# Optimization experiments

Hardware: AMD Instinct MI355X
Metric: run time of the kernel (lower is better)

Reference implementation:

```python
import jax, jax.numpy as jnp
import numpy as np

B, S, N, D = 4, 12, 716, 64
H = 4            # num_heads
ALPHA = 0.2      # LeakyReLU negative slope
NEG = -9e15      # mask fill value from the torch code (-9000000000000000.0)


def setup_inputs() -> dict:
    key = jax.random.key(0)
    ks = jax.random.split(key, 20)
    sc = 1.0 / np.sqrt(D)
    inputs = jax.random.normal(ks[0], (B, S, N, D), dtype=jnp.float32)
    adj = jax.random.randint(ks[1], (N, N), 0, 2).astype(jnp.int32)
    in_degree = jax.random.randint(ks[2], (N,), 0, N)
    out_degree = jax.random.randint(ks[3], (N,), 0, N)
    # embeddings with padding_idx=0 -> row 0 zeroed
    in_emb = (jax.random.normal(ks[4], (N, D)) * sc).at[0].set(0.0)
    out_emb = (jax.random.normal(ks[5], (N, D)) * sc).at[0].set(0.0)
    # GAT params
    W = jax.random.normal(ks[6], (D, D)) * sc
    a1 = jax.random.normal(ks[7], (D, 1)) * sc
    a2 = jax.random.normal(ks[8], (D, 1)) * sc
    # spatial multi-head attention params
    Wq = jax.random.normal(ks[9], (D, D)) * sc
    bq = jnp.zeros((D,))
    Wk = jax.random.normal(ks[10], (D, D)) * sc
    bk = jnp.zeros((D,))
    Wv = jax.random.normal(ks[11], (D, D)) * sc
    bv = jnp.zeros((D,))
    Wo = jax.random.normal(ks[12], (D, D)) * sc
    bo = jnp.zeros((D,))
    # pred_linear: 2D -> D
    Wp = jax.random.normal(ks[13], (2 * D, D)) * (1.0 / np.sqrt(2 * D))
    bp = jnp.zeros((D,))
    return dict(inputs=inputs, adj=adj, in_degree=in_degree, out_degree=out_degree,
                in_emb=in_emb, out_emb=out_emb, W=W, a1=a1, a2=a2,
                Wq=Wq, bq=bq, Wk=Wk, bk=bk, Wv=Wv, bv=bv, Wo=Wo, bo=bo,
                Wp=Wp, bp=bp)


def reference(inputs, adj, in_degree, out_degree, in_emb, out_emb,
              W, a1, a2, Wq, bq, Wk, bk, Wv, bv, Wo, bo, Wp, bp):
    b, s, n, d = inputs.shape
    dh = d // H
    # degree embeddings, broadcast over batch & time: [N, D]
    spatial_emb = in_emb[in_degree] + out_emb[out_degree]

    # ---- GAT, vectorized over all batch*seq samples (orig loops per sample) ----
    x = inputs.reshape(b * s, n, d)
    Wh = jnp.einsum('bnd,de->bne', x, W)                 # [BS, N, D]
    Wh1 = Wh @ a1                                        # [BS, N, 1]
    Wh2 = Wh @ a2                                        # [BS, N, 1]
    e = Wh1 + jnp.swapaxes(Wh2, 1, 2)                    # [BS, N, N]
    e = jnp.where(e > 0, e, ALPHA * e)                   # LeakyReLU
    e = jnp.where(adj[None] > 0, e, NEG)                 # adjacency mask
    attn = jax.nn.softmax(e, axis=-1)                    # softmax(dim=1) on 2D == last axis
    out1 = jax.nn.elu(attn @ Wh).reshape(b, s, n, d)     # dropout is identity in eval

    # ---- Spatial multi-head attention over nodes ----
    y = inputs + spatial_emb                             # [B, S, N, D]
    q = (y @ Wq + bq).reshape(b, s, n, H, dh)
    k = (y @ Wk + bk).reshape(b, s, n, H, dh)
    v = (y @ Wv + bv).reshape(b, s, n, H, dh)
    scores = jnp.einsum('bsnhk,bsmhk->bshnm', q, k) / jnp.sqrt(jnp.float32(dh))
    p = jax.nn.softmax(scores, axis=-1)                  # [B, S, H, N, N]
    o = jnp.einsum('bshnm,bsmhk->bsnhk', p, v).reshape(b, s, n, d)
    out2 = o @ Wo + bo

    # ---- fuse and project ----
    return jnp.concatenate([out1, out2], axis=-1) @ Wp + bp
```

## Files before the change

### kernel.cpp

```cpp
#include <hip/hip_runtime.h>
#include <hip/hip_bf16.h>

#define BN   716
#define BD   64
#define BH   4
#define BDH  16
#define BBS  48
#define NCH  23
#define NJT  45
#define QSCALE 0.3606737602f

typedef __hip_bfloat16 bf16;
typedef __attribute__((ext_vector_type(8))) short short8;
typedef __attribute__((ext_vector_type(4))) short s16x4;
typedef __attribute__((ext_vector_type(4))) float f32x4;

__device__ __forceinline__ float b2f(bf16 x){ return __bfloat162float(x); }
__device__ __forceinline__ bf16 f2b(float x){ return __float2bfloat16(x); }
__device__ __forceinline__ short bfbits(float x){
  union { bf16 h; short s; } c; c.h = __float2bfloat16(x); return c.s;
}
__device__ __forceinline__ unsigned packbf(float a, float b){
  unsigned ua = __float_as_uint(a) + 0x8000u;
  unsigned ub = __float_as_uint(b) + 0x8000u;
  return __builtin_amdgcn_perm(ub, ua, 0x07060302u);
}
__device__ __forceinline__ short8 pack8(float a,float b,float c,float d,
                                        float e,float f,float g,float h){
  short8 r; r[0]=bfbits(a); r[1]=bfbits(b); r[2]=bfbits(c); r[3]=bfbits(d);
  r[4]=bfbits(e); r[5]=bfbits(f); r[6]=bfbits(g); r[7]=bfbits(h); return r;
}
__device__ __forceinline__ float fexp2(float x){
#if __has_builtin(__builtin_amdgcn_exp2f)
  return __builtin_amdgcn_exp2f(x);
#else
  return __expf(x * 0.6931471805599453f);
#endif
}
__device__ __forceinline__ float frcp(float x){
#if __has_builtin(__builtin_amdgcn_rcpf)
  return __builtin_amdgcn_rcpf(x);
#else
  return 1.0f / x;
#endif
}

#define MFMA16(a,b,c) __builtin_amdgcn_mfma_f32_16x16x32_bf16(a,b,c,0,0,0)

#if __has_builtin(__builtin_amdgcn_mfma_f32_16x16x16_bf16)
#define HAVE_MFMA16K 1
__device__ __forceinline__ f32x4 mfma16k(s16x4 a, s16x4 b, f32x4 c){
  return __builtin_amdgcn_mfma_f32_16x16x16_bf16(a, b, c, 0, 0, 0);
}
#elif __has_builtin(__builtin_amdgcn_mfma_f32_16x16x16bf16_1k)
#define HAVE_MFMA16K 1
__device__ __forceinline__ f32x4 mfma16k(s16x4 a, s16x4 b, f32x4 c){
  return __builtin_amdgcn_mfma_f32_16x16x16bf16_1k(a, b, c, 0, 0, 0);
}
#else
#define HAVE_MFMA16K 0
#endif

__global__ __launch_bounds__(256) void k_prep(
    const int* __restrict__ adj,
    const float* __restrict__ W,  const float* __restrict__ Wq,
    const float* __restrict__ Wk, const float* __restrict__ Wv,
    const float* __restrict__ Wo, const float* __restrict__ bo,
    const float* __restrict__ Wp, const float* __restrict__ bp,
    unsigned* __restrict__ mask, bf16* __restrict__ WB,
    bf16* __restrict__ WF, float* __restrict__ bfuse)
{
  int b = blockIdx.x, t = threadIdx.x;
  if (b < 65){
    int w = b * 256 + t;
    if (w < BN * NCH){
      int row = w / NCH, wc = w - row * NCH;
      unsigned m = 0;
      int jb = wc * 32;
      for (int bb = 0; bb < 32; bb++){
        int j = jb + bb;
        if (j < BN && adj[(long)row * BN + j] > 0) m |= (1u << bb);
      }
      mask[w] = m;
    }
  } else if (b < 69){
#pragma unroll
    for (int i = 0; i < 16; i++){
      int idx = (b - 65) * 4096 + i * 256 + t;
      int n = idx >> 6, kk = idx & 63;
      const float* src = (n < 64) ? W : (n < 128) ? Wq : (n < 192) ? Wk : Wv;
      WB[idx] = f2b(src[kk * BD + (n & 63)]);
    }
  } else if (b < 101){
    int idx = (b - 69) * 256 + t;
    int n = idx >> 7, kk = idx & 127;
    float v;
    if (kk < 64){
      v = Wp[kk * BD + n];
    } else {
      v = 0.f;
      int r = kk - 64;
      for (int m = 0; m < BD; m++)
        v += Wo[r * BD + m] * Wp[(BD + m) * BD + n];
    }
    WF[idx] = f2b(v);
  } else {
    if (t < BD){
      float acc = bp[t];
      for (int m = 0; m < BD; m++)
        acc += bo[m] * Wp[(BD + m) * BD + t];
      bfuse[t] = acc;
    }
  }
}

__global__ __launch_bounds__(256) void k_proj(
    const float* __restrict__ x,
    const int* __restrict__ ind, const int* __restrict__ outd,
    const float* __restrict__ in_emb, const float* __restrict__ out_emb,
    const float* __restrict__ a1p, const float* __restrict__ a2p,
    const bf16* __restrict__ WB,
    const float* __restrict__ bq, const float* __restrict__ bk, const float* __restrict__ bv,
    bf16* __restrict__ WhS, float* __restrict__ Wh1, float2* __restrict__ EwP,
    bf16* __restrict__ Qt, bf16* __restrict__ Kt, bf16* __restrict__ Vt16)
{
  __shared__ short st[64][72];
  int bs = blockIdx.x, tile = blockIdx.y;
  int n0 = tile * 64;
  int t = threadIdx.x, w = t >> 6, lane = t & 63, quad = lane >> 4, l15 = lane & 15;
  long sb = (long)bs * BN;
  int rowi = n0 + w * 16 + l15;
  int rc = rowi < BN ? rowi : BN - 1;
  const float* xr  = x + (sb + rc) * BD;
  const float* ier = in_emb  + (long)ind [rc] * BD;
  const float* oer = out_emb + (long)outd[rc] * BD;

  f32x4 aw[4], aqkv[12];
#pragma unroll
  for (int i2 = 0; i2 < 4;  i2++) aw[i2]   = (f32x4){0,0,0,0};
#pragma unroll
  for (int i2 = 0; i2 < 12; i2++) aqkv[i2] = (f32x4){0,0,0,0};

#pragma unroll
  for (int kc = 0; kc < 2; kc++){
    int k0 = kc * 32 + quad * 8;
    float4 xa = *(const float4*)(xr  + k0);
    float4 xb = *(const float4*)(xr  + k0 + 4);
    float4 ia = *(const float4*)(ier + k0);
    float4 ib = *(const float4*)(ier + k0 + 4);
    float4 oa = *(const float4*)(oer + k0);
    float4 ob = *(const float4*)(oer + k0 + 4);
    short8 ax = pack8(xa.x, xa.y, xa.z, xa.w, xb.x, xb.y, xb.z, xb.w);
    short8 ay = pack8(xa.x+ia.x+oa.x, xa.y+ia.y+oa.y, xa.z+ia.z+oa.z, xa.w+ia.w+oa.w,
                      xb.x+ib.x+ob.x, xb.y+ib.y+ob.y, xb.z+ib.z+ob.z, xb.w+ib.w+ob.w);
#pragma unroll
    for (int nt = 0; nt < 4; nt++)
      aw[nt] = MFMA16(ax, *(const short8*)(WB + (nt*16 + l15) * BD + k0), aw[nt]);
#pragma unroll
    for (int nt = 0; nt < 12; nt++)
      aqkv[nt] = MFMA16(ay, *(const short8*)(WB + (64 + nt*16 + l15) * BD + k0), aqkv[nt]);
  }

  {
    float s1v[4] = {0,0,0,0}, s2v[4] = {0,0,0,0};
#pragma unroll
    for (int nt = 0; nt < 4; nt++){
      float a1f = a1p[nt*16 + l15], a2f = a2p[nt*16 + l15];
#pragma unroll
      for (int reg = 0; reg < 4; reg++){
        s1v[reg] += aw[nt][reg] * a1f;
        s2v[reg] += aw[nt][reg] * a2f;
      }
    }
#pragma unroll
    for (int off = 1; off < 16; off <<= 1){
#pragma unroll
      for (int reg = 0; reg < 4; reg++){
        s1v[reg] += __shfl_xor(s1v[reg], off);
        s2v[reg] += __shfl_xor(s2v[reg], off);
      }
    }
    if (l15 == 0){
#pragma unroll
      for (int reg = 0; reg < 4; reg++){
        int rr = n0 + w*16 + quad*4 + reg;
        if (rr < BN){
          Wh1[sb + rr] = s1v[reg];
          float s2 = s2v[reg];
          EwP[sb + rr] = make_float2(__expf(s2), __expf(0.2f * s2));
        }
      }
    }
  }

#pragma unroll
  for (int nt = 0; nt < 4; nt++)
    *(short4*)&st[nt*16 + l15][w*16 + quad*4] = make_short4(
        bfbits(aw[nt][0]), bfbits(aw[nt][1]), bfbits(aw[nt][2]), bfbits(aw[nt][3]));
  __syncthreads();
#pragma unroll
  for (int s = 0; s < 2; s++){
    int L = (t*2 + s) * 8;
    int kb = L & 31, d = (L >> 5) & 63, chl = L >> 11;
    int ch = tile * 2 + chl;
    if (ch < NCH)
      *(uint4*)(WhS + (((long)bs*NCH + ch)*64 + d)*32 + kb) = *(const uint4*)&st[d][chl*32 + kb];
  }
  __syncthreads();

#pragma unroll
  for (int nt = 0; nt < 4; nt++){
    float bb = bv[nt*16 + l15];
    *(short4*)&st[nt*16 + l15][w*16 + quad*4] = make_short4(
        bfbits(aqkv[8+nt][0]+bb), bfbits(aqkv[8+nt][1]+bb),
        bfbits(aqkv[8+nt][2]+bb), bfbits(aqkv[8+nt][3]+bb));
  }
  __syncthreads();
  {
    int jl = t >> 6;
    int c  = t & 15, qq = (t >> 4) & 3;
    int jt = tile * 4 + jl;
    if (jt < NJT){
#pragma unroll
      for (int h = 0; h < BH; h++){
        s16x4 v4 = *(const s16x4*)&st[h*16 + c][jl*16 + qq*4];
        *(s16x4*)(Vt16 + ((((long)bs*BH + h)*NJT + jt)*64 + (t & 63))*4) = v4;
      }
    }
  }
  __syncthreads();

#pragma unroll
  for (int nt = 0; nt < 4; nt++){
    float bb = bq[nt*16 + l15];
#pragma unroll
    for (int reg = 0; reg < 4; reg++)
      st[w*16 + quad*4 + reg][nt*16 + l15] = bfbits((aqkv[nt][reg] + bb) * QSCALE);
  }
  __syncthreads();
#pragma unroll
  for (int s = 0; s < 2; s++){
    int L = (t*2 + s) * 8;
    int kb = L & 15, nl = (L >> 4) & 63, h = L >> 10;
    int jt = tile * 4 + (nl >> 4);
    if (jt < NJT)
      *(uint4*)(Qt + ((((long)bs*BH + h)*NJT + jt)*16 + (nl&15))*16 + kb)
          = *(const uint4*)&st[nl][h*16 + kb];
  }
  __syncthreads();

#pragma unroll
  for (int nt = 0; nt < 4; nt++){
    float bb = bk[nt*16 + l15];
#pragma unroll
    for (int reg = 0; reg < 4; reg++)
      st[w*16 + quad*4 + reg][nt*16 + l15] = bfbits(aqkv[4+nt][reg] + bb);
  }
  __syncthreads();
#pragma unroll
  for (int s = 0; s < 2; s++){
    int L = (t*2 + s) * 8;
    int kb = L & 15, nl = (L >> 4) & 63, h = L >> 10;
    int jt = tile * 4 + (nl >> 4);
    if (jt < NJT)
      *(uint4*)(Kt + ((((long)bs*BH + h)*NJT + jt)*16 + (nl&15))*16 + kb)
          = *(const uint4*)&st[nl][h*16 + kb];
  }
}

__global__ __launch_bounds__(256) void k_attn(
    const float* __restrict__ Wh1, const float2* __restrict__ EwP,
    const unsigned* __restrict__ mask, const bf16* __restrict__ WhS,
    const bf16* __restrict__ Qt, const bf16* __restrict__ Kt,
    const bf16* __restrict__ Vt16,
    bf16* __restrict__ out1, bf16* __restrict__ o)
{
#if !HAVE_MFMA16K
  __shared__ short pw[4][16][48];
#endif
  int bs = blockIdx.x, yb = blockIdx.y;
  int t = threadIdx.x, w = t >> 6, lane = t & 63, quad = lane >> 4, l15 = lane & 15;
  long sb = (long)bs * BN;

  if (yb < 12){
    int rt = yb * 4 + w;
    if (rt >= NJT) return;
    int i = rt * 16 + l15;
    int ic = i < BN ? i : BN - 1;
    float e1 = Wh1[sb + ic];
    float Aa = __expf(e1), Cc = __expf(0.2f * e1);
    float invA = frcp(Aa);
    const unsigned* mrow = mask + (long)ic * NCH;
    const float2* ew = EwP + sb;

    float sl = 0.f;
    f32x4 acc0 = {0,0,0,0}, acc1 = {0,0,0,0}, acc2 = {0,0,0,0}, acc3 = {0,0,0,0};
    for (int ch = 0; ch < NCH; ch++){
      int j0 = ch * 32 + quad * 8;
      unsigned m8 = (mrow[ch] >> (quad * 8)) & 0xFFu;
      const float4* ef = (const float4*)(ew + j0);
      float4 q0 = ef[0], q1 = ef[1], q2 = ef[2], q3 = ef[3];
      float Bv[8] = {q0.x, q0.z, q1.x, q1.z, q2.x, q2.z, q3.x, q3.z};
      float Dv[8] = {q0.y, q0.w, q1.y, q1.w, q2.y, q2.w, q3.y, q3.w};
      float p[8];
#pragma unroll
      for (int jj = 0; jj < 8; jj++){
        bool cond = Bv[jj] > invA;
        float f = cond ? Bv[jj] : Dv[jj];
        float g = cond ? Aa : Cc;
        float pp = ((m8 >> jj) & 1u) ? f * g : 0.f;
        sl += pp;
        p[jj] = pp;
      }
      union { unsigned u[4]; short8 v; } A;
      A.u[0] = packbf(p[0], p[1]); A.u[1] = packbf(p[2], p[3]);
      A.u[2] = packbf(p[4], p[5]); A.u[3] = packbf(p[6], p[7]);
      const bf16* wbp = WhS + ((long)bs*NCH + ch)*2048 + quad * 8;
      acc0 = MFMA16(A.v, *(const short8*)(wbp + ( 0 + l15) * 32), acc0);
      acc1 = MFMA16(A.v, *(const short8*)(wbp + (16 + l15) * 32), acc1);
      acc2 = MFMA16(A.v, *(const short8*)(wbp + (32 + l15) * 32), acc2);
      acc3 = MFMA16(A.v, *(const short8*)(wbp + (48 + l15) * 32), acc3);
    }
    sl += __shfl_xor(sl, 16);
    sl += __shfl_xor(sl, 32);
    float inv[4];
#pragma unroll
    for (int reg = 0; reg < 4; reg++){
      int srcl = quad * 4 + reg;
      float s = __int_as_float(__builtin_amdgcn_ds_bpermute(srcl << 2, __float_as_int(sl)));
      inv[reg] = 1.0f / s;
    }
    const f32x4* accs[4] = {&acc0, &acc1, &acc2, &acc3};
#pragma unroll
    for (int nt = 0; nt < 4; nt++){
#pragma unroll
      for (int reg = 0; reg < 4; reg++){
        int gi = rt * 16 + quad * 4 + reg;
        if (gi < BN){
          float val = (*accs[nt])[reg] * inv[reg];
          val = (val > 0.f) ? val : (__expf(val) - 1.f);
          out1[(sb + gi) * BD + nt*16 + l15] = f2b(val);
        }
      }
    }
    return;
  }

  int h = w;
  int rt0 = (yb - 12) * 2, rt1 = rt0 + 1;
  const bf16* Qh = Qt   + ((long)bs*BH + h) * NJT * 256;
  const bf16* Kh = Kt   + ((long)bs*BH + h) * NJT * 256;
  const bf16* Vh = Vt16 + ((long)bs*BH + h) * NJT * 256;

  short8 aq0 = {0,0,0,0,0,0,0,0}, aq1 = {0,0,0,0,0,0,0,0};
  if (quad < 2){
    aq0 = *(const short8*)(Qh + rt0*256 + l15*16 + quad*8);
    aq1 = *(const short8*)(Qh + rt1*256 + l15*16 + quad*8);
  }
  f32x4 o0 = {0,0,0,0}, o1 = {0,0,0,0};
  float ps0 = 0.f, ps1 = 0.f;

#if HAVE_MFMA16K
  auto step = [&](int jt, bool tail){
    short8 ak = {0,0,0,0,0,0,0,0};
    if (quad < 2) ak = *(const short8*)(Kh + jt*256 + l15*16 + quad*8);
    f32x4 c0 = MFMA16(ak, aq0, ((f32x4){0,0,0,0}));
    f32x4 c1 = MFMA16(ak, aq1, ((f32x4){0,0,0,0}));
    float p0[4], p1[4];
#pragma unroll
    for (int reg = 0; reg < 4; reg++){
      float a = fexp2(c0[reg]);
      float b = fexp2(c1[reg]);
      if (tail && quad == 3){ a = 0.f; b = 0.f; }
      ps0 += a; ps1 += b;
      p0[reg] = a; p1[reg] = b;
    }
    union { unsigned u[2]; s16x4 v; } A0, A1;
    A0.u[0] = packbf(p0[0], p0[1]); A0.u[1] = packbf(p0[2], p0[3]);
    A1.u[0] = packbf(p1[0], p1[1]); A1.u[1] = packbf(p1[2], p1[3]);
    s16x4 bv = *(const s16x4*)(Vh + jt*256 + lane*4);
    o0 = mfma16k(A0.v, bv, o0);
    o1 = mfma16k(A1.v, bv, o1);
  };
  for (int jt = 0; jt < NJT - 1; jt++) step(jt, false);
  step(NJT - 1, true);
#else
  for (int pass = 0; pass < 2; pass++){
    int rt = pass ? rt1 : rt0;
    short8 aq = pass ? aq1 : aq0;
    f32x4 oacc = {0,0,0,0};
    float psum = 0.f;
    if (rt < NJT){
      for (int ch = 0; ch < NCH; ch++){
#pragma unroll
        for (int tt = 0; tt < 2; tt++){
          int jt = 2*ch + tt;
          if (jt < NJT){
            short8 ak = {0,0,0,0,0,0,0,0};
            if (quad < 2) ak = *(const short8*)(Kh + jt*256 + l15*16 + quad*8);
            f32x4 c = MFMA16(ak, aq, ((f32x4){0,0,0,0}));
            bool inval = (jt == NJT-1) && (quad == 3);
#pragma unroll
            for (int reg = 0; reg < 4; reg++){
              float pp = fexp2(c[reg]);
              pp = inval ? 0.f : pp;
              psum += pp;
              pw[h][l15][tt*16 + quad*4 + reg] = (short)((__float_as_uint(pp) + 0x8000u) >> 16);
            }
          } else {
#pragma unroll
            for (int reg = 0; reg < 4; reg++) pw[h][l15][tt*16 + quad*4 + reg] = 0;
          }
        }
        short8 ap = *(const short8*)&pw[h][l15][quad*8];
        int jB = 2*ch + (quad >> 1);
        s16x4 v0 = {0,0,0,0}, v1 = {0,0,0,0};
        if (jB < NJT){
          v0 = *(const s16x4*)(Vh + jB*256 + (((quad&1)*2  )*16 + l15)*4);
          v1 = *(const s16x4*)(Vh + jB*256 + (((quad&1)*2+1)*16 + l15)*4);
        }
        short8 bv8; bv8[0]=v0[0]; bv8[1]=v0[1]; bv8[2]=v0[2]; bv8[3]=v0[3];
        bv8[4]=v1[0]; bv8[5]=v1[1]; bv8[6]=v1[2]; bv8[7]=v1[3];
        oacc = MFMA16(ap, bv8, oacc);
      }
    }
    if (pass){ o1 = oacc; ps1 = psum; } else { o0 = oacc; ps0 = psum; }
  }
#endif

  ps0 += __shfl_xor(ps0, 16); ps0 += __shfl_xor(ps0, 32);
  ps1 += __shfl_xor(ps1, 16); ps1 += __shfl_xor(ps1, 32);
#pragma unroll
  for (int reg = 0; reg < 4; reg++){
    int srcl = quad * 4 + reg;
    float s0 = __int_as_float(__builtin_amdgcn_ds_bpermute(srcl << 2, __float_as_int(ps0)));
    float s1 = __int_as_float(__builtin_amdgcn_ds_bpermute(srcl << 2, __float_as_int(ps1)));
    int g0 = rt0 * 16 + srcl;
    int g1 = rt1 * 16 + srcl;
    if (g0 < BN) o[(sb + g0) * BD + h * BDH + l15] = f2b(o0[reg] / s0);
    if (g1 < BN) o[(sb + g1) * BD + h * BDH + l15] = f2b(o1[reg] / s1);
  }
}

__global__ __launch_bounds__(256) void k_final(
    const bf16* __restrict__ out1, const bf16* __restrict__ o,
    const bf16* __restrict__ WF, const float* __restrict__ bfuse,
    float* __restrict__ out)
{
  int t = threadIdx.x, w = t >> 6, lane = t & 63, quad = lane >> 4, l15 = lane & 15;
  long r0 = (long)blockIdx.x * 64;
  long row = r0 + w * 16 + l15;
  const bf16* o1r = out1 + row * BD;
  const bf16* oor = o    + row * BD;
  f32x4 acc[4];
#pragma unroll
  for (int i2 = 0; i2 < 4; i2++) acc[i2] = (f32x4){0,0,0,0};
#pragma unroll
  for (int kc = 0; kc < 2; kc++){
    int k0 = kc * 32 + quad * 8;
    short8 a1 = *(const short8*)(o1r + k0);
    short8 a2 = *(const short8*)(oor + k0);
#pragma unroll
    for (int nt = 0; nt < 4; nt++){
      acc[nt] = MFMA16(a1, *(const short8*)(WF + (nt*16 + l15) * 128 + k0), acc[nt]);
      acc[nt] = MFMA16(a2, *(const short8*)(WF + (nt*16 + l15) * 128 + 64 + k0), acc[nt]);
    }
  }
#pragma unroll
  for (int nt = 0; nt < 4; nt++){
    float bf = bfuse[nt*16 + l15];
#pragma unroll
    for (int reg = 0; reg < 4; reg++)
      out[(r0 + w*16 + quad*4 + reg) * BD + nt*16 + l15] = acc[nt][reg] + bf;
  }
}

extern "C" void kernel_launch(void* const* d_in, const int* in_sizes, int n_in,
                              void* d_out, int out_size, void* d_ws, size_t ws_size,
                              hipStream_t stream){
  const float* inp    = (const float*)d_in[0];
  const int*   adj    = (const int*)  d_in[1];
  const int*   ind    = (const int*)  d_in[2];
  const int*   outd   = (const int*)  d_in[3];
  const float* in_emb = (const float*)d_in[4];
  const float* out_emb= (const float*)d_in[5];
  const float* W      = (const float*)d_in[6];
  const float* a1     = (const float*)d_in[7];
  const float* a2     = (const float*)d_in[8];
  const float* Wq     = (const float*)d_in[9];
  const float* bq     = (const float*)d_in[10];
  const float* Wk     = (const float*)d_in[11];
  const float* bk     = (const float*)d_in[12];
  const float* Wv     = (const float*)d_in[13];
  const float* bv     = (const float*)d_in[14];
  const float* Wo     = (const float*)d_in[15];
  const float* bo     = (const float*)d_in[16];
  const float* Wp     = (const float*)d_in[17];
  const float* bp     = (const float*)d_in[18];

  const long PER  = (long)BBS * BN * BD;
  const long WHS  = (long)BBS * NCH * 64 * 32;
  const long QTS  = (long)BBS * BH * NJT * 16 * 16;
  bf16* WhSb  = (bf16*)d_ws;
  bf16* Vt16b = WhSb  + WHS;
  bf16* Qtb   = Vt16b + QTS;
  bf16* Ktb   = Qtb   + QTS;
  bf16* o1B   = Ktb   + QTS;
  bf16* oB    = o1B + PER;
  bf16* WBb   = oB  + PER;
  bf16* WFb   = WBb + 256 * BD;
  unsigned* maskb = (unsigned*)(WFb + BD * 128);
  float2* EwPb = (float2*)(maskb + BN * NCH);
  float* fws  = (float*)(EwPb + (long)BBS * BN + 32);
  float* Wh1  = fws;
  float* bfuse= Wh1 + (long)BBS * BN + 64;

  hipLaunchKernelGGL(k_prep, dim3(102), dim3(256), 0, stream,
                     adj, W, Wq, Wk, Wv, Wo, bo, Wp, bp,
                     maskb, WBb, WFb, bfuse);
  hipLaunchKernelGGL(k_proj, dim3(BBS, 12), dim3(256), 0, stream,
                     inp, ind, outd, in_emb, out_emb, a1, a2, WBb, bq, bk, bv,
                     WhSb, Wh1, EwPb, Qtb, Ktb, Vt16b);
  hipLaunchKernelGGL(k_attn, dim3(BBS, 35), dim3(256), 0, stream,
                     Wh1, EwPb, maskb, WhSb, Qtb, Ktb, Vt16b, o1B, oB);
  hipLaunchKernelGGL(k_final, dim3(537), dim3(256), 0, stream,
                     o1B, oB, WFb, bfuse, (float*)d_out);
}
```

Baseline: 178.6 us.

## Split spatial attention to one row tile per block and cut proj syncs

In k_proj, four separate shared-memory staging buffers replace the single reused one, so the Wh, V, Q and K tiles are written together behind one barrier instead of being staged one after another with about seven barriers. In k_attn, each spatial-attention block now handles one query row tile instead of two, and the grid grows from 35 to 57 in y to expose more parallel blocks. The QK^T score step now uses a 16x16x16 MFMA with 4-wide loads instead of a zero-padded 8-wide MFMA. This trades K/V reuse across two row tiles and more shared memory per block in k_proj for more parallelism and fewer barriers.

```diff
diff --git a/kernel.cpp b/kernel.cpp
--- a/kernel.cpp
+++ b/kernel.cpp
@@ -124,7 +124,10 @@
     bf16* __restrict__ WhS, float* __restrict__ Wh1, float2* __restrict__ EwP,
     bf16* __restrict__ Qt, bf16* __restrict__ Kt, bf16* __restrict__ Vt16)
 {
-  __shared__ short st[64][72];
+  __shared__ short stA[64][72];
+  __shared__ short stB[64][72];
+  __shared__ short stC[64][72];
+  __shared__ short stD[64][72];
   int bs = blockIdx.x, tile = blockIdx.y;
   int n0 = tile * 64;
   int t = threadIdx.x, w = t >> 6, lane = t & 63, quad = lane >> 4, l15 = lane & 15;
@@ -194,28 +197,31 @@
   }
 
 #pragma unroll
-  for (int nt = 0; nt < 4; nt++)
-    *(short4*)&st[nt*16 + l15][w*16 + quad*4] = make_short4(
+  for (int nt = 0; nt < 4; nt++){
+    *(short4*)&stA[nt*16 + l15][w*16 + quad*4] = make_short4(
         bfbits(aw[nt][0]), bfbits(aw[nt][1]), bfbits(aw[nt][2]), bfbits(aw[nt][3]));
+    float bb = bv[nt*16 + l15];
+    *(short4*)&stB[nt*16 + l15][w*16 + quad*4] = make_short4(
+        bfbits(aqkv[8+nt][0]+bb), bfbits(aqkv[8+nt][1]+bb),
+        bfbits(aqkv[8+nt][2]+bb), bfbits(aqkv[8+nt][3]+bb));
+    float bq_ = bq[nt*16 + l15];
+    float bk_ = bk[nt*16 + l15];
+#pragma unroll
+    for (int reg = 0; reg < 4; reg++){
+      stC[w*16 + quad*4 + reg][nt*16 + l15] = bfbits((aqkv[nt][reg] + bq_) * QSCALE);
+      stD[w*16 + quad*4 + reg][nt*16 + l15] = bfbits(aqkv[4+nt][reg] + bk_);
+    }
+  }
   __syncthreads();
+
 #pragma unroll
   for (int s = 0; s < 2; s++){
     int L = (t*2 + s) * 8;
     int kb = L & 31, d = (L >> 5) & 63, chl = L >> 11;
     int ch = tile * 2 + chl;
     if (ch < NCH)
-      *(uint4*)(WhS + (((long)bs*NCH + ch)*64 + d)*32 + kb) = *(const uint4*)&st[d][chl*32 + kb];
-  }
-  __syncthreads();
-
-#pragma unroll
-  for (int nt = 0; nt < 4; nt++){
-    float bb = bv[nt*16 + l15];
-    *(short4*)&st[nt*16 + l15][w*16 + quad*4] = make_short4(
-        bfbits(aqkv[8+nt][0]+bb), bfbits(aqkv[8+nt][1]+bb),
-        bfbits(aqkv[8+nt][2]+bb), bfbits(aqkv[8+nt][3]+bb));
-  }
-  __syncthreads();
+      *(uint4*)(WhS + (((long)bs*NCH + ch)*64 + d)*32 + kb) = *(const uint4*)&stA[d][chl*32 + kb];
+  }
   {
     int jl = t >> 6;
     int c  = t & 15, qq = (t >> 4) & 3;
@@ -223,48 +229,22 @@
     if (jt < NJT){
 #pragma unroll
       for (int h = 0; h < BH; h++){
-        s16x4 v4 = *(const s16x4*)&st[h*16 + c][jl*16 + qq*4];
+        s16x4 v4 = *(const s16x4*)&stB[h*16 + c][jl*16 + qq*4];
         *(s16x4*)(Vt16 + ((((long)bs*BH + h)*NJT + jt)*64 + (t & 63))*4) = v4;
       }
     }
   }
-  __syncthreads();
-
-#pragma unroll
-  for (int nt = 0; nt < 4; nt++){
-    float bb = bq[nt*16 + l15];
-#pragma unroll
-    for (int reg = 0; reg < 4; reg++)
-      st[w*16 + quad*4 + reg][nt*16 + l15] = bfbits((aqkv[nt][reg] + bb) * QSCALE);
-  }
-  __syncthreads();
 #pragma unroll
   for (int s = 0; s < 2; s++){
     int L = (t*2 + s) * 8;
     int kb = L & 15, nl = (L >> 4) & 63, h = L >> 10;
     int jt = tile * 4 + (nl >> 4);
-    if (jt < NJT)
+    if (jt < NJT){
       *(uint4*)(Qt + ((((long)bs*BH + h)*NJT + jt)*16 + (nl&15))*16 + kb)
-          = *(const uint4*)&st[nl][h*16 + kb];
-  }
-  __syncthreads();
-
-#pragma unroll
-  for (int nt = 0; nt < 4; nt++){
-    float bb = bk[nt*16 + l15];
-#pragma unroll
-    for (int reg = 0; reg < 4; reg++)
-      st[w*16 + quad*4 + reg][nt*16 + l15] = bfbits(aqkv[4+nt][reg] + bb);
-  }
-  __syncthreads();
-#pragma unroll
-  for (int s = 0; s < 2; s++){
-    int L = (t*2 + s) * 8;
-    int kb = L & 15, nl = (L >> 4) & 63, h = L >> 10;
-    int jt = tile * 4 + (nl >> 4);
-    if (jt < NJT)
+          = *(const uint4*)&stC[nl][h*16 + kb];
       *(uint4*)(Kt + ((((long)bs*BH + h)*NJT + jt)*16 + (nl&15))*16 + kb)
-          = *(const uint4*)&st[nl][h*16 + kb];
+          = *(const uint4*)&stD[nl][h*16 + kb];
+    }
   }
 }
 
@@ -346,99 +326,94 @@
     return;
   }
 
-  int h = w;
-  int rt0 = (yb - 12) * 2, rt1 = rt0 + 1;
+  int h = w, rt = yb - 12;
   const bf16* Qh = Qt   + ((long)bs*BH + h) * NJT * 256;
   const bf16* Kh = Kt   + ((long)bs*BH + h) * NJT * 256;
   const bf16* Vh = Vt16 + ((long)bs*BH + h) * NJT * 256;
 
-  short8 aq0 = {0,0,0,0,0,0,0,0}, aq1 = {0,0,0,0,0,0,0,0};
-  if (quad < 2){
-    aq0 = *(const short8*)(Qh + rt0*256 + l15*16 + quad*8);
-    aq1 = *(const short8*)(Qh + rt1*256 + l15*16 + quad*8);
-  }
-  f32x4 o0 = {0,0,0,0}, o1 = {0,0,0,0};
-  float ps0 = 0.f, ps1 = 0.f;
+  f32x4 oacc = {0,0,0,0};
+  float psum = 0.f;
 
 #if HAVE_MFMA16K
-  auto step = [&](int jt, bool tail){
-    short8 ak = {0,0,0,0,0,0,0,0};
-    if (quad < 2) ak = *(const short8*)(Kh + jt*256 + l15*16 + quad*8);
-    f32x4 c0 = MFMA16(ak, aq0, ((f32x4){0,0,0,0}));
-    f32x4 c1 = MFMA16(ak, aq1, ((f32x4){0,0,0,0}));
-    float p0[4], p1[4];
+  s16x4 bq16 = *(const s16x4*)(Qh + rt*256 + l15*16 + quad*4);
+#pragma unroll 4
+  for (int jt = 0; jt < NJT - 1; jt++){
+    s16x4 ak = *(const s16x4*)(Kh + jt*256 + l15*16 + quad*4);
+    f32x4 c = mfma16k(ak, bq16, ((f32x4){0,0,0,0}));
+    float p[4];
 #pragma unroll
     for (int reg = 0; reg < 4; reg++){
-      float a = fexp2(c0[reg]);
-      float b = fexp2(c1[reg]);
-      if (tail && quad == 3){ a = 0.f; b = 0.f; }
-      ps0 += a; ps1 += b;
-      p0[reg] = a; p1[reg] = b;
-    }
-    union { unsigned u[2]; s16x4 v; } A0, A1;
-    A0.u[0] = packbf(p0[0], p0[1]); A0.u[1] = packbf(p0[2], p0[3]);
-    A1.u[0] = packbf(p1[0], p1[1]); A1.u[1] = packbf(p1[2], p1[3]);
+      float pp = fexp2(c[reg]);
+      psum += pp;
+      p[reg] = pp;
+    }
+    union { unsigned u[2]; s16x4 v; } A;
+    A.u[0] = packbf(p[0], p[1]); A.u[1] = packbf(p[2], p[3]);
     s16x4 bv = *(const s16x4*)(Vh + jt*256 + lane*4);
-    o0 = mfma16k(A0.v, bv, o0);
-    o1 = mfma16k(A1.v, bv, o1);
-  };
-  for (int jt = 0; jt < NJT - 1; jt++) step(jt, false);
-  step(NJT - 1, true);
+    oacc = mfma16k(A.v, bv, oacc);
+  }
+  {
+    int jt = NJT - 1;
+    s16x4 ak = *(const s16x4*)(Kh + jt*256 + l15*16 + quad*4);
+    f32x4 c = mfma16k(ak, bq16, ((f32x4){0,0,0,0}));
+    float p[4];
+#pragma unroll
+    for (int reg = 0; reg < 4; reg++){
+      float pp = (quad == 3) ? 0.f : fexp2(c[reg]);
+      psum += pp;
+      p[reg] = pp;
+    }
+    union { unsigned u[2]; s16x4 v; } A;
+    A.u[0] = packbf(p[0], p[1]); A.u[1] = packbf(p[2], p[3]);
+    s16x4 bv = *(const s16x4*)(Vh + jt*256 + lane*4);
+    oacc = mfma16k(A.v, bv, oacc);
+  }
 #else
-  for (int pass = 0; pass < 2; pass++){
-    int rt = pass ? rt1 : rt0;
-    short8 aq = pass ? aq1 : aq0;
-    f32x4 oacc = {0,0,0,0};
-    float psum = 0.f;
-    if (rt < NJT){
-      for (int ch = 0; ch < NCH; ch++){
-#pragma unroll
-        for (int tt = 0; tt < 2; tt++){
-          int jt = 2*ch + tt;
-          if (jt < NJT){
-            short8 ak = {0,0,0,0,0,0,0,0};
-            if (quad < 2) ak = *(const short8*)(Kh + jt*256 + l15*16 + quad*8);
-            f32x4 c = MFMA16(ak, aq, ((f32x4){0,0,0,0}));
-            bool inval = (jt == NJT-1) && (quad == 3);
-#pragma unroll
-            for (int reg = 0; reg < 4; reg++){
-              float pp = fexp2(c[reg]);
-              pp = inval ? 0.f : pp;
-              psum += pp;
-              pw[h][l15][tt*16 + quad*4 + reg] = (short)((__float_as_uint(pp) + 0x8000u) >> 16);
-            }
-          } else {
-#pragma unroll
-            for (int reg = 0; reg < 4; reg++) pw[h][l15][tt*16 + quad*4 + reg] = 0;
-          }
+  short8 aq = {0,0,0,0,0,0,0,0};
+  if (quad < 2) aq = *(const short8*)(Qh + rt*256 + l15*16 + quad*8);
+  for (int ch = 0; ch < NCH; ch++){
+#pragma unroll
+    for (int tt = 0; tt < 2; tt++){
+      int jt = 2*ch + tt;
+      if (jt < NJT){
+        short8 ak = {0,0,0,0,0,0,0,0};
+        if (quad < 2) ak = *(const short8*)(Kh + jt*256 + l15*16 + quad*8);
+        f32x4 c = MFMA16(ak, aq, ((f32x4){0,0,0,0}));
+        bool inval = (jt == NJT-1) && (quad == 3);
+#pragma unroll
+        for (int reg = 0; reg < 4; reg++){
+          float pp = fexp2(c[reg]);
+          pp = inval ? 0.f : pp;
+          psum += pp;
+          pw[h][l15][tt*16 + quad*4 + reg] = (short)((__float_as_uint(pp) + 0x8000u) >> 16);
         }
-        short8 ap = *(const short8*)&pw[h][l15][quad*8];
-        int jB = 2*ch + (quad >> 1);
-        s16x4 v0 = {0,0,0,0}, v1 = {0,0,0,0};
-        if (jB < NJT){
-          v0 = *(const s16x4*)(Vh + jB*256 + (((quad&1)*2  )*16 + l15)*4);
-          v1 = *(const s16x4*)(Vh + jB*256 + (((quad&1)*2+1)*16 + l15)*4);
-        }
-        short8 bv8; bv8[0]=v0[0]; bv8[1]=v0[1]; bv8[2]=v0[2]; bv8[3]=v0[3];
-        bv8[4]=v1[0]; bv8[5]=v1[1]; bv8[6]=v1[2]; bv8[7]=v1[3];
-        oacc = MFMA16(ap, bv8, oacc);
-      }
-    }
-    if (pass){ o1 = oacc; ps1 = psum; } else { o0 = oacc; ps0 = psum; }
+      } else {
+#pragma unroll
+        for (int reg = 0; reg < 4; reg++) pw[h][l15][tt*16 + quad*4 + reg] = 0;
+      }
+    }
+    short8 ap = *(const short8*)&pw[h][l15][quad*8];
+    int jB = 2*ch + (quad >> 1);
+    s16x4 v0 = {0,0,0,0}, v1 = {0,0,0,0};
+    if (jB < NJT){
+      v0 = *(const s16x4*)(Vh + jB*256 + (((quad&1)*2  )*16 + l15)*4);
+      v1 = *(const s16x4*)(Vh + jB*256 + (((quad&1)*2+1)*16 + l15)*4);
+    }
+    short8 bv8; bv8[0]=v0[0]; bv8[1]=v0[1]; bv8[2]=v0[2]; bv8[3]=v0[3];
+    bv8[4]=v1[0]; bv8[5]=v1[1]; bv8[6]=v1[2]; bv8[7]=v1[3];
+    oacc = MFMA16(ap, bv8, oacc);
   }
 #endif
 
-  ps0 += __shfl_xor(ps0, 16); ps0 += __shfl_xor(ps0, 32);
-  ps1 += __shfl_xor(ps1, 16); ps1 += __shfl_xor(ps1, 32);
+  psum += __shfl_xor(psum, 16);
+  psum += __shfl_xor(psum, 32);
 #pragma unroll
   for (int reg = 0; reg < 4; reg++){
     int srcl = quad * 4 + reg;
-    float s0 = __int_as_float(__builtin_amdgcn_ds_bpermute(srcl << 2, __float_as_int(ps0)));
-    float s1 = __int_as_float(__builtin_amdgcn_ds_bpermute(srcl << 2, __float_as_int(ps1)));
-    int g0 = rt0 * 16 + srcl;
-    int g1 = rt1 * 16 + srcl;
-    if (g0 < BN) o[(sb + g0) * BD + h * BDH + l15] = f2b(o0[reg] / s0);
-    if (g1 < BN) o[(sb + g1) * BD + h * BDH + l15] = f2b(o1[reg] / s1);
+    float s = __int_as_float(__builtin_amdgcn_ds_bpermute(srcl << 2, __float_as_int(psum)));
+    int grow = rt * 16 + srcl;
+    if (grow < BN)
+      o[(sb + grow) * BD + h * BDH + l15] = f2b(oacc[reg] / s);
   }
 }
 
@@ -521,7 +496,7 @@
   hipLaunchKernelGGL(k_proj, dim3(BBS, 12), dim3(256), 0, stream,
                      inp, ind, outd, in_emb, out_emb, a1, a2, WBb, bq, bk, bv,
                      WhSb, Wh1, EwPb, Qtb, Ktb, Vt16b);
-  hipLaunchKernelGGL(k_attn, dim3(BBS, 35), dim3(256), 0, stream,
+  hipLaunchKernelGGL(k_attn, dim3(BBS, 57), dim3(256), 0, stream,
                      Wh1, EwPb, maskb, WhSb, Qtb, Ktb, Vt16b, o1B, oB);
   hipLaunchKernelGGL(k_final, dim3(537), dim3(256), 0, stream,
                      o1B, oB, WFb, bfuse, (float*)d_out);
```

New measurement: 180.1 us. Within noise of the previous version (+0.8%).
